# Kernel tuning notes

Measured on AMD Instinct MI355X. Metric: run time of the kernel, lower is better.

Reference implementation:

```python
import jax, jax.numpy as jnp
import numpy as np
from jax import lax

SCORE_THRESHOLD = 0.01
NMS_THRESHOLD = 0.5
MAX_DETECTIONS = 100
PRE_NMS_TOPK = 512  # fixed-shape candidate pool per class (tf NMS is unbounded; 512 >> max_detections covers it)
NEG_INF = -jnp.inf


def setup_inputs() -> dict:
    key = jax.random.key(0)
    k1, k2, k3, k4, k5 = jax.random.split(key, 5)
    B, N, C = 32, 50000, 10
    # valid (x1,y1,x2,y2) boxes: random top-left + positive width/height
    xy = jax.random.uniform(k1, (B, N, 2), dtype=jnp.float32) * 500.0
    wh = jax.random.uniform(k2, (B, N, 2), dtype=jnp.float32) * 100.0 + 1.0
    boxes = jnp.concatenate([xy, xy + wh], axis=-1)
    classification = jax.random.uniform(k3, (B, N, C), dtype=jnp.float32)
    rotation = jax.random.normal(k4, (B, N, 3), dtype=jnp.float32)
    translation = jax.random.normal(k5, (B, N, 3), dtype=jnp.float32)
    return {"boxes": boxes, "classification": classification,
            "rotation": rotation, "translation": translation}


def _iou_matrix(b):  # b: (K,4) in (x1,y1,x2,y2)
    x1, y1, x2, y2 = b[:, 0], b[:, 1], b[:, 2], b[:, 3]
    area = (x2 - x1) * (y2 - y1)  # (K,)
    ix1 = jnp.maximum(x1[:, None], x1[None, :])
    iy1 = jnp.maximum(y1[:, None], y1[None, :])
    ix2 = jnp.minimum(x2[:, None], x2[None, :])
    iy2 = jnp.minimum(y2[:, None], y2[None, :])
    inter = jnp.maximum(ix2 - ix1, 0.0) * jnp.maximum(iy2 - iy1, 0.0)
    union = area[:, None] + area[None, :] - inter
    return jnp.where(union > 0.0, inter / union, 0.0)  # (K,K)


def _greedy_nms_keep(iou, valid):
    # iou: (K,K) for boxes already sorted by descending score; valid: (K,) bool
    K = iou.shape[0]
    def body(suppressed, xs):
        iou_row, valid_i, i = xs
        keep_i = valid_i & jnp.logical_not(suppressed[i])
        suppressed = jnp.where(keep_i, suppressed | (iou_row > NMS_THRESHOLD), suppressed)
        return suppressed, keep_i
    _, keep = lax.scan(body, jnp.zeros((K,), bool), (iou, valid, jnp.arange(K)))
    return keep


def _per_class(scores, boxes_i):
    # scores: (N,), boxes_i: (N,4) -> kept candidate scores (K,) (-inf where dropped) and anchor idx (K,)
    sc = jnp.where(scores > SCORE_THRESHOLD, scores, NEG_INF)
    vals, idx = lax.top_k(sc, PRE_NMS_TOPK)          # sorted desc
    valid = vals > SCORE_THRESHOLD                    # also false for -inf pads
    iou = _iou_matrix(boxes_i[idx])
    keep = _greedy_nms_keep(iou, valid)
    keep = keep & (jnp.cumsum(keep.astype(jnp.int32)) <= MAX_DETECTIONS)
    return jnp.where(keep, vals, NEG_INF), idx


def _per_image(boxes_i, cls_i, rot_i, trans_i):
    # boxes_i (N,4), cls_i (N,C), rot_i (N,3), trans_i (N,3)
    C = cls_i.shape[1]
    sc_ck, idx_ck = jax.vmap(_per_class, in_axes=(1, None))(cls_i, boxes_i)  # (C,K)
    labels_ck = jnp.broadcast_to(jnp.arange(C, dtype=jnp.int32)[:, None], sc_ck.shape)
    sc_flat = sc_ck.reshape(-1)
    idx_flat = idx_ck.reshape(-1)
    lab_flat = labels_ck.reshape(-1)
    top_scores, sel = lax.top_k(sc_flat, MAX_DETECTIONS)   # global top-k across classes
    sel_idx = idx_flat[sel]
    sel_lab = lab_flat[sel]
    valid = jnp.isfinite(top_scores)
    out_boxes = jnp.where(valid[:, None], boxes_i[sel_idx], -1.0)
    out_scores = jnp.where(valid, top_scores, -1.0)
    out_labels = jnp.where(valid, sel_lab, -1).astype(jnp.int32)
    out_rot = jnp.where(valid[:, None], rot_i[sel_idx], -1.0)
    out_trans = jnp.where(valid[:, None], trans_i[sel_idx], -1.0)
    return out_boxes, out_scores, out_labels, out_rot, out_trans


def reference(boxes, classification, rotation, translation):
    return jax.vmap(_per_image)(boxes, classification, rotation, translation)
```

## Files before the change

kernel.cpp:

```cpp
#include <hip/hip_runtime.h>
#include <math.h>

typedef unsigned int u32;
typedef unsigned long long u64;

constexpr int NB   = 32;
constexpr int NN   = 50000;
constexpr int NC   = 10;
constexpr int KK   = 512;
constexpr int MAXD = 100;
constexpr int CAP  = 2048;
constexpr int LCAP = 192;
constexpr int GCH  = 2500;
constexpr int KMAX = 1024;
constexpr u32 TBIN = 252;
constexpr int RLIM = 192;

constexpr int OFF_BOX = 0;
constexpr int OFF_SC  = NB * MAXD * 4;
constexpr int OFF_LB  = OFF_SC + NB * MAXD;
constexpr int OFF_RT  = OFF_LB + NB * MAXD;
constexpr int OFF_TR  = OFF_RT + NB * MAXD * 3;

__device__ __forceinline__ u32 ord_f32(float s) {
  u32 u = __float_as_uint(s);
  return (u & 0x80000000u) ? ~u : (u | 0x80000000u);
}
__device__ __forceinline__ float unord_f32(u32 o) {
  u32 u = (o & 0x80000000u) ? (o & 0x7FFFFFFFu) : ~o;
  return __uint_as_float(u);
}
__device__ __forceinline__ u64 make_key(float s, u32 i) {
  float sp = (s > 0.01f) ? s : -INFINITY;
  return ((u64)ord_f32(sp) << 32) | (u64)(u32)(~i);
}
__device__ __forceinline__ u32 digest16(float x) {
  if (!(x > 0.01f)) return 0;
  u32 q = (u32)(x * 65536.0f);
  return q > 65535u ? 65535u : q;
}
__device__ __forceinline__ float readlane_f(float v, int lane) {
  return __int_as_float(__builtin_amdgcn_readlane(__float_as_int(v), lane));
}
__device__ __forceinline__ u64 readlane_u64(u64 v, int lane) {
  u32 lo = __builtin_amdgcn_readlane((u32)v, lane);
  u32 hi = __builtin_amdgcn_readlane((u32)(v >> 32), lane);
  return ((u64)hi << 32) | lo;
}
__device__ __forceinline__ int clamp_idx(int idx) {
  return idx < 0 ? 0 : (idx >= NN ? NN - 1 : idx);
}

__global__ __launch_bounds__(512) void gather_kernel(
    const float* __restrict__ cls, u64* __restrict__ glist,
    u32* __restrict__ gcnt) {
  const int blk = blockIdx.x;
  const int b = blk / 20, ch = blk % 20;
  const float* src = cls + (size_t)b * NN * NC + (size_t)ch * GCH * NC;
  __shared__ u32 lcnt[NC];
  __shared__ u32 lbase[NC];
  __shared__ u64 lbuf[NC][LCAP];
  const int t = threadIdx.x;
  if (t < NC) lcnt[t] = 0;
  __syncthreads();
  for (int q = t; q < GCH * NC / 4; q += 512) {
    float4 v = ((const float4*)src)[q];
    float arr[4] = {v.x, v.y, v.z, v.w};
#pragma unroll
    for (int k = 0; k < 4; ++k) {
      int e = q * 4 + k;
      int c = e % 10;
      float x = arr[k];
      if ((digest16(x) >> 8) >= TBIN) {
        u32 idx = (u32)((ch * (GCH * NC) + e) / 10);
        u32 p = atomicAdd(&lcnt[c], 1u);
        if (p < (u32)LCAP) {
          lbuf[c][p] = make_key(x, idx);
        } else {
          u32 g = atomicAdd(&gcnt[b * NC + c], 1u);
          if (g < (u32)CAP) glist[(size_t)(b * NC + c) * CAP + g] = make_key(x, idx);
        }
      }
    }
  }
  __syncthreads();
  if (t < NC) {
    u32 n = min(lcnt[t], (u32)LCAP);
    lbase[t] = atomicAdd(&gcnt[b * NC + t], n);
  }
  __syncthreads();
  for (int c = 0; c < NC; ++c) {
    u32 n = min(lcnt[c], (u32)LCAP);
    u32 base = lbase[c];
    for (u32 i = t; i < n; i += 512) {
      u32 p = base + i;
      if (p < (u32)CAP) glist[(size_t)(b * NC + c) * CAP + p] = lbuf[c][i];
    }
  }
}

__global__ __launch_bounds__(512) void sort_kernel(
    const float* __restrict__ cls, const u64* __restrict__ glist,
    const u32* __restrict__ gcnt, const float* __restrict__ boxes,
    u64* __restrict__ selg, float4* __restrict__ bxg) {
  __shared__ __align__(16) unsigned char smem[16448];
  u64* cand = (u64*)smem;
  ushort (*prank)[8] = (ushort(*)[8])(smem + 8192);
  __shared__ int s_cnt, s_d;
  const int p = blockIdx.x >> 1, half = blockIdx.x & 1;
  const int bc = (p & 7) * 40 + (p >> 3);
  const int b = bc / NC;
  const int t = threadIdx.x, lane = t & 63, wv = t >> 6;

  int M = (int)gcnt[bc];
  const bool fast = (M >= KK && M <= KMAX);
  if (fast) {
    for (int i = t; i < KMAX; i += 512)
      cand[i] = (i < M) ? glist[(size_t)bc * CAP + i] : (u64)i;
  } else {
    const int c = bc % NC;
    const float* sbase = cls + (size_t)b * NN * NC + c;
    u32* hist = (u32*)smem;
    for (int i = t; i < 4096; i += 512) hist[i] = 0;
    if (t == 0) s_cnt = 0;
    __syncthreads();
    for (int i = t; i < NN; i += 512)
      atomicAdd(&hist[digest16(sbase[(size_t)i * NC]) >> 4], 1u);
    __syncthreads();
    if (t == 0) {
      u32 run = 0, d = 1;
      for (int i = 4095; i >= 1; --i) {
        run += hist[i];
        if (run >= (u32)KK) { d = (u32)i; break; }
        d = 1;
      }
      s_d = (int)d;
    }
    __syncthreads();
    const u32 dstar = (u32)s_d;
    for (int i = t; i < KMAX; i += 512) cand[i] = (u64)i;
    __syncthreads();
    for (int i = t; i < NN; i += 512) {
      float x = sbase[(size_t)i * NC];
      u32 dg = digest16(x) >> 4;
      if (dg >= dstar && dg >= 1) {
        int pq = atomicAdd(&s_cnt, 1);
        if (pq < KMAX) cand[pq] = make_key(x, (u32)i);
      }
    }
    __syncthreads();
    M = min(s_cnt, KMAX);
  }

  u64 ck0 = 0;
  float4 pb0;
  if (fast) {
    ck0 = cand[half * 512 + t];
    const int pidx = clamp_idx((int)(~(u32)ck0));
    pb0 = *(const float4*)(boxes + ((size_t)b * NN + pidx) * 4);
  }
  __syncthreads();

  const int h2lo = fast ? half : 0;
  const int h2hi = fast ? half : 1;
  for (int h2 = h2lo; h2 <= h2hi; ++h2) {
    {
      u64 myk[8];
#pragma unroll
      for (int k = 0; k < 8; ++k) myk[k] = cand[h2 * 512 + lane + k * 64];
      int rnk[8];
#pragma unroll
      for (int k = 0; k < 8; ++k) rnk[k] = 0;
      const int j0 = wv * 128;
      const int rem = M - j0;
      const int jjmax = rem <= 0 ? 0 : (rem >= 128 ? 64 : ((rem + 1) >> 1));
      for (int jj = 0; jj < jjmax; ++jj) {
        const ulonglong2 v = *(const ulonglong2*)&cand[j0 + jj * 2];
#pragma unroll
        for (int k = 0; k < 8; ++k) {
          rnk[k] += (v.x > myk[k]) ? 1 : 0;
          rnk[k] += (v.y > myk[k]) ? 1 : 0;
        }
      }
#pragma unroll
      for (int k = 0; k < 8; ++k) prank[lane + k * 64][wv] = (ushort)rnk[k];
    }
    __syncthreads();
    {
      const uint4 pv = *(const uint4*)&prank[t][0];
      const int r = (int)(pv.x & 0xFFFFu) + (int)(pv.x >> 16) +
                    (int)(pv.y & 0xFFFFu) + (int)(pv.y >> 16) +
                    (int)(pv.z & 0xFFFFu) + (int)(pv.z >> 16) +
                    (int)(pv.w & 0xFFFFu) + (int)(pv.w >> 16);
      const int ig = h2 * 512 + t;
      if (ig < M && r < KK) {
        const u64 key = fast ? ck0 : cand[ig];
        selg[(size_t)bc * KK + r] = key;
        if (fast) {
          bxg[(size_t)bc * KK + r] = pb0;
        } else {
          const int pidx = clamp_idx((int)(~(u32)key));
          bxg[(size_t)bc * KK + r] =
              *(const float4*)(boxes + ((size_t)b * NN + pidx) * 4);
        }
      }
    }
    if (h2 < h2hi) __syncthreads();
  }
  if (M < KK) {
    for (int r = M + t; r < KK; r += 512) {
      selg[(size_t)bc * KK + r] = make_key(-INFINITY, 0);
      bxg[(size_t)bc * KK + r] =
          *(const float4*)(boxes + ((size_t)b * NN + 0) * 4);
    }
  }
}

__global__ __launch_bounds__(512) void nms_kernel(
    const u64* __restrict__ selg, const float4* __restrict__ bxg,
    int* __restrict__ tidx, float* __restrict__ ksc) {
  __shared__ __align__(16) unsigned char smem[26560];
  float4* bx4 = (float4*)smem;
  float* ars = (float*)(smem + 8192);
  float* sscore = (float*)(smem + 10240);
  u64 (*rowm)[9] = (u64(*)[9])(smem + 12288);
  u64* kmask = (u64*)(smem + 26432);
  const int bc = (blockIdx.x & 7) * 40 + (blockIdx.x >> 3);
  const int t = threadIdx.x, lane = t & 63, wv = t >> 6;

  {
    const u64 k = selg[(size_t)bc * KK + t];
    tidx[bc * KK + t] = clamp_idx((int)(~(u32)k));
    const float4 bx = bxg[(size_t)bc * KK + t];
    bx4[t] = bx;
    ars[t] = (bx.z - bx.x) * (bx.w - bx.y);
    sscore[t] = unord_f32((u32)(k >> 32));
  }
  __syncthreads();

  float jx1[8], jy1[8], jx2[8], jy2[8], jar[8];
#pragma unroll
  for (int q = 0; q < 8; ++q) {
    const float4 bb = bx4[q * 64 + lane];
    jx1[q] = bb.x; jy1[q] = bb.y; jx2[q] = bb.z; jy2[q] = bb.w;
    jar[q] = ars[q * 64 + lane];
  }


#pragma unroll
  for (int g = 0; g < RLIM / 64; ++g) {
    for (int rr = 0; rr < 8; ++rr) {
      const int il = wv + 8 * rr;
      const int i = g * 64 + il;
      const float bix1 = readlane_f(jx1[g], il);
      const float biy1 = readlane_f(jy1[g], il);
      const float bix2 = readlane_f(jx2[g], il);
      const float biy2 = readlane_f(jy2[g], il);
      const float bia  = readlane_f(jar[g], il);
      u64 m[8];
#pragma unroll
      for (int q = 0; q < 8; ++q) {
        m[q] = 0;
        if (q >= g) {
          float ix1 = fmaxf(bix1, jx1[q]);
          float iy1 = fmaxf(biy1, jy1[q]);
          float ix2 = fminf(bix2, jx2[q]);
          float iy2 = fminf(biy2, jy2[q]);
          float iw = fmaxf(ix2 - ix1, 0.0f);
          float ih = fmaxf(iy2 - iy1, 0.0f);
          float inter = iw * ih;
          float uni = bia + jar[q] - inter;
          bool s = (uni > 0.0f) && ((inter - 0.5f * uni) > uni * 0x1p-25f);
          m[q] = __ballot(s);
        }
      }
      u64 word = m[0];
#pragma unroll
      for (int q = 1; q < 8; ++q) word = (lane == q) ? m[q] : word;
      if (lane < 8) rowm[i][lane] = word;
    }
  }
  __syncthreads();

  if (wv == 0) {
    u64 vw_[8], kw[8];
#pragma unroll
    for (int q = 0; q < 8; ++q) {
      const float sc = sscore[q * 64 + lane];
      vw_[q] = __ballot(sc > 0.01f);
      kw[q] = 0;
    }
    u64 vsup = 0;
    int count = 0;
    bool done = false;
#pragma unroll
    for (int w = 0; w < 8; ++w) {
      if (!done) {
        u64 av = vw_[w] & ~readlane_u64(vsup, w);
        while (av) {
          const int bbit = (int)__builtin_ctzll(av);
          const int i = w * 64 + bbit;
          kw[w] |= 1ull << bbit;
          if (++count == MAXD) { done = true; break; }
          if (w < RLIM / 64) {
            const u64 row = (lane < 8) ? rowm[i][lane] : 0;
            vsup |= row;
          } else {
            const float bix1 = readlane_f(jx1[w], bbit);
            const float biy1 = readlane_f(jy1[w], bbit);
            const float bix2 = readlane_f(jx2[w], bbit);
            const float biy2 = readlane_f(jy2[w], bbit);
            const float bia  = readlane_f(jar[w], bbit);
            u64 m[8];
#pragma unroll
            for (int q = 0; q < 8; ++q) {
              m[q] = 0;
              if (q >= w) {
                float ix1 = fmaxf(bix1, jx1[q]);
                float iy1 = fmaxf(biy1, jy1[q]);
                float ix2 = fminf(bix2, jx2[q]);
                float iy2 = fminf(biy2, jy2[q]);
                float iw = fmaxf(ix2 - ix1, 0.0f);
                float ih = fmaxf(iy2 - iy1, 0.0f);
                float inter = iw * ih;
                float uni = bia + jar[q] - inter;
                bool s = (uni > 0.0f) && ((inter - 0.5f * uni) > uni * 0x1p-25f);
                m[q] = __ballot(s);
              }
            }
            u64 word = m[0];
#pragma unroll
            for (int q = 1; q < 8; ++q) word = (lane == q) ? m[q] : word;
            vsup |= word;
          }
          const u64 mask_gt = (bbit == 63) ? 0ull : (~0ull << (bbit + 1));
          av = vw_[w] & ~readlane_u64(vsup, w) & mask_gt;
        }
      }
    }
    if (lane < 8) {
      u64 word = kw[0];
#pragma unroll
      for (int q = 1; q < 8; ++q) word = (lane == q) ? kw[q] : word;
      kmask[lane] = word;
    }
  }
  __syncthreads();
  {
    const float sc = sscore[t];
    const bool keep = (kmask[t >> 6] >> (t & 63)) & 1ull;
    ksc[(size_t)bc * KK + t] = keep ? sc : -INFINITY;
  }
}

__global__ __launch_bounds__(512) void final_kernel(
    const float* __restrict__ boxes, const float* __restrict__ rot,
    const float* __restrict__ trans, const int* __restrict__ tidx,
    const float* __restrict__ ksc, float* __restrict__ out) {
  const int b = blockIdx.x;
  __shared__ __align__(16) u64 ck[KMAX];
  __shared__ __align__(16) ushort prank[KMAX][8];
  __shared__ u64 top[MAXD];
  __shared__ int cnt;
  const int t = threadIdx.x;
  const int lane = t & 63, wv = t >> 6;
  if (t == 0) cnt = 0;
  if (t < MAXD) top[t] = make_key(-INFINITY, 0);
  for (int i = t; i < KMAX; i += 512) ck[i] = (u64)i;
  __syncthreads();
  for (int j = t; j < NC * KK; j += 512) {
    float s = ksc[b * NC * KK + j];
    if (s != -INFINITY) {
      int p = atomicAdd(&cnt, 1);
      if (p < KMAX) ck[p] = ((u64)ord_f32(s) << 32) | (u64)(u32)(~(u32)j);
    }
  }
  __syncthreads();
  const int n = min(cnt, KMAX);
  {
    u64 myk[16];
#pragma unroll
    for (int k = 0; k < 16; ++k) myk[k] = ck[lane + k * 64];
    int rnk[16];
#pragma unroll
    for (int k = 0; k < 16; ++k) rnk[k] = 0;
    const int j0 = wv * 128;
    const int rem = n - j0;
    const int jjmax = rem <= 0 ? 0 : (rem >= 128 ? 64 : ((rem + 1) >> 1));
    for (int jj = 0; jj < jjmax; ++jj) {
      const ulonglong2 v = *(const ulonglong2*)&ck[j0 + jj * 2];
#pragma unroll
      for (int k = 0; k < 16; ++k) {
        rnk[k] += (v.x > myk[k]) ? 1 : 0;
        rnk[k] += (v.y > myk[k]) ? 1 : 0;
      }
    }
#pragma unroll
    for (int k = 0; k < 16; ++k) prank[lane + k * 64][wv] = (ushort)rnk[k];
  }
  __syncthreads();
#pragma unroll
  for (int h = 0; h < 2; ++h) {
    const int i = h * 512 + t;
    const uint4 pv = *(const uint4*)&prank[i][0];
    const int r = (int)(pv.x & 0xFFFFu) + (int)(pv.x >> 16) +
                  (int)(pv.y & 0xFFFFu) + (int)(pv.y >> 16) +
                  (int)(pv.z & 0xFFFFu) + (int)(pv.z >> 16) +
                  (int)(pv.w & 0xFFFFu) + (int)(pv.w >> 16);
    if (i < n && r < MAXD) top[r] = ck[i];
  }
  __syncthreads();

  if (t < MAXD) {
    float b0 = -1.f, b1 = -1.f, b2 = -1.f, b3 = -1.f;
    float os = -1.f, ol = -1.f;
    float r0 = -1.f, r1 = -1.f, r2 = -1.f;
    float t0 = -1.f, t1 = -1.f, t2 = -1.f;
    const u64 k = top[t];
    const float sc = unord_f32((u32)(k >> 32));
    if (sc != -INFINITY) {
      int j = (int)(~(u32)k);
      int c = j >> 9, slot = j & (KK - 1);
      int idx = tidx[(b * NC + c) * KK + slot];
      os = sc;
      ol = (float)c;
      const float4 bx = *(const float4*)(boxes + ((size_t)b * NN + idx) * 4);
      b0 = bx.x; b1 = bx.y; b2 = bx.z; b3 = bx.w;
      const float* rp = rot + ((size_t)b * NN + idx) * 3;
      r0 = rp[0]; r1 = rp[1]; r2 = rp[2];
      const float* tp = trans + ((size_t)b * NN + idx) * 3;
      t0 = tp[0]; t1 = tp[1]; t2 = tp[2];
    }
    const int o = b * MAXD + t;
    out[OFF_BOX + (size_t)o * 4 + 0] = b0;
    out[OFF_BOX + (size_t)o * 4 + 1] = b1;
    out[OFF_BOX + (size_t)o * 4 + 2] = b2;
    out[OFF_BOX + (size_t)o * 4 + 3] = b3;
    out[OFF_SC + o] = os;
    out[OFF_LB + o] = ol;
    out[OFF_RT + (size_t)o * 3 + 0] = r0;
    out[OFF_RT + (size_t)o * 3 + 1] = r1;
    out[OFF_RT + (size_t)o * 3 + 2] = r2;
    out[OFF_TR + (size_t)o * 3 + 0] = t0;
    out[OFF_TR + (size_t)o * 3 + 1] = t1;
    out[OFF_TR + (size_t)o * 3 + 2] = t2;
  }
}

extern "C" void kernel_launch(void* const* d_in, const int* in_sizes, int n_in,
                              void* d_out, int out_size, void* d_ws, size_t ws_size,
                              hipStream_t stream) {
  const float* boxes = (const float*)d_in[0];
  const float* cls   = (const float*)d_in[1];
  const float* rot   = (const float*)d_in[2];
  const float* trans = (const float*)d_in[3];
  float* out = (float*)d_out;

  u64* glist   = (u64*)d_ws;
  u64* selg    = glist + (size_t)NB * NC * CAP;
  float4* bxg  = (float4*)(selg + (size_t)NB * NC * KK);
  int* tidx    = (int*)(bxg + (size_t)NB * NC * KK);
  float* ksc   = (float*)(tidx + NB * NC * KK);
  u32* gcnt    = (u32*)(ksc + NB * NC * KK);

  hipMemsetAsync(gcnt, 0, NB * NC * sizeof(u32), stream);
  gather_kernel<<<NB * 20, 512, 0, stream>>>(cls, glist, gcnt);
  sort_kernel<<<NB * NC * 2, 512, 0, stream>>>(cls, glist, gcnt, boxes, selg, bxg);
  nms_kernel<<<NB * NC, 512, 0, stream>>>(selg, bxg, tidx, ksc);
  final_kernel<<<NB, 512, 0, stream>>>(boxes, rot, trans, tidx, ksc, out);
}
```

Baseline: 111.0 us.

## Replace global atomic compaction with fixed per-chunk segments and drop memset

The gather kernel now writes each chunk's per-class candidates into a fixed 96-slot segment and records a per-chunk count, marking overflow with a sentinel, so global atomics are no longer needed. The sort kernel computes prefix offsets from the 20 chunk counts and compacts the segments into shared memory, falling back to the slow histogram path when any chunk overflows. This removes the hipMemsetAsync launch and global atomic contention. In exchange the sort kernel issues more scattered loads and takes the slow path more often if chunk counts exceed the segment size.

Result: no change. 112.7 us (+1.5%).

```diff
diff --git a/kernel.cpp b/kernel.cpp
--- a/kernel.cpp
+++ b/kernel.cpp
@@ -10,11 +10,13 @@
 constexpr int KK   = 512;
 constexpr int MAXD = 100;
 constexpr int CAP  = 2048;
+constexpr int SEGC = 96;
 constexpr int LCAP = 192;
 constexpr int GCH  = 2500;
 constexpr int KMAX = 1024;
 constexpr u32 TBIN = 252;
 constexpr int RLIM = 192;
+constexpr u32 SENT = 0xFFFFu;
 
 constexpr int OFF_BOX = 0;
 constexpr int OFF_SC  = NB * MAXD * 4;
@@ -53,12 +55,11 @@
 
 __global__ __launch_bounds__(512) void gather_kernel(
     const float* __restrict__ cls, u64* __restrict__ glist,
-    u32* __restrict__ gcnt) {
+    u32* __restrict__ gcnt2) {
   const int blk = blockIdx.x;
   const int b = blk / 20, ch = blk % 20;
   const float* src = cls + (size_t)b * NN * NC + (size_t)ch * GCH * NC;
   __shared__ u32 lcnt[NC];
-  __shared__ u32 lbase[NC];
   __shared__ u64 lbuf[NC][LCAP];
   const int t = threadIdx.x;
   if (t < NC) lcnt[t] = 0;
@@ -74,34 +75,26 @@
       if ((digest16(x) >> 8) >= TBIN) {
         u32 idx = (u32)((ch * (GCH * NC) + e) / 10);
         u32 p = atomicAdd(&lcnt[c], 1u);
-        if (p < (u32)LCAP) {
-          lbuf[c][p] = make_key(x, idx);
-        } else {
-          u32 g = atomicAdd(&gcnt[b * NC + c], 1u);
-          if (g < (u32)CAP) glist[(size_t)(b * NC + c) * CAP + g] = make_key(x, idx);
-        }
+        if (p < (u32)LCAP) lbuf[c][p] = make_key(x, idx);
       }
     }
   }
   __syncthreads();
   if (t < NC) {
-    u32 n = min(lcnt[t], (u32)LCAP);
-    lbase[t] = atomicAdd(&gcnt[b * NC + t], n);
+    u32 n = lcnt[t];
+    gcnt2[(size_t)(b * 20 + ch) * NC + t] = (n > (u32)SEGC) ? SENT : n;
   }
   __syncthreads();
   for (int c = 0; c < NC; ++c) {
-    u32 n = min(lcnt[c], (u32)LCAP);
-    u32 base = lbase[c];
-    for (u32 i = t; i < n; i += 512) {
-      u32 p = base + i;
-      if (p < (u32)CAP) glist[(size_t)(b * NC + c) * CAP + p] = lbuf[c][i];
-    }
+    u32 n = min(lcnt[c], (u32)SEGC);
+    for (u32 i = t; i < n; i += 512)
+      glist[(size_t)(b * NC + c) * CAP + ch * SEGC + i] = lbuf[c][i];
   }
 }
 
 __global__ __launch_bounds__(512) void sort_kernel(
     const float* __restrict__ cls, const u64* __restrict__ glist,
-    const u32* __restrict__ gcnt, const float* __restrict__ boxes,
+    const u32* __restrict__ gcnt2, const float* __restrict__ boxes,
     u64* __restrict__ selg, float4* __restrict__ bxg) {
   __shared__ __align__(16) unsigned char smem[16448];
   u64* cand = (u64*)smem;
@@ -109,16 +102,30 @@
   __shared__ int s_cnt, s_d;
   const int p = blockIdx.x >> 1, half = blockIdx.x & 1;
   const int bc = (p & 7) * 40 + (p >> 3);
-  const int b = bc / NC;
+  const int b = bc / NC, c = bc % NC;
   const int t = threadIdx.x, lane = t & 63, wv = t >> 6;
 
-  int M = (int)gcnt[bc];
-  const bool fast = (M >= KK && M <= KMAX);
+  u32 cnts[20];
+  int pre[20];
+  int M = 0;
+  bool bad = false;
+#pragma unroll
+  for (int s = 0; s < 20; ++s) {
+    u32 n = gcnt2[(size_t)(b * 20 + s) * NC + c];
+    cnts[s] = n;
+    pre[s] = M;
+    if (n == SENT) bad = true; else M += (int)n;
+  }
+  const bool fast = (!bad && M >= KK && M <= KMAX);
   if (fast) {
-    for (int i = t; i < KMAX; i += 512)
-      cand[i] = (i < M) ? glist[(size_t)bc * CAP + i] : (u64)i;
+    for (int i = t; i < KMAX; i += 512) cand[i] = (u64)i;
+    __syncthreads();
+#pragma unroll
+    for (int s = 0; s < 20; ++s) {
+      if (t < (int)cnts[s])
+        cand[pre[s] + t] = glist[(size_t)bc * CAP + s * SEGC + t];
+    }
   } else {
-    const int c = bc % NC;
     const float* sbase = cls + (size_t)b * NN * NC + c;
     u32* hist = (u32*)smem;
     for (int i = t; i < 4096; i += 512) hist[i] = 0;
@@ -151,6 +158,7 @@
     __syncthreads();
     M = min(s_cnt, KMAX);
   }
+  __syncthreads();
 
   u64 ck0 = 0;
   float4 pb0;
@@ -159,7 +167,6 @@
     const int pidx = clamp_idx((int)(~(u32)ck0));
     pb0 = *(const float4*)(boxes + ((size_t)b * NN + pidx) * 4);
   }
-  __syncthreads();
 
   const int h2lo = fast ? half : 0;
   const int h2hi = fast ? half : 1;
@@ -461,11 +468,10 @@
   float4* bxg  = (float4*)(selg + (size_t)NB * NC * KK);
   int* tidx    = (int*)(bxg + (size_t)NB * NC * KK);
   float* ksc   = (float*)(tidx + NB * NC * KK);
-  u32* gcnt    = (u32*)(ksc + NB * NC * KK);
-
-  hipMemsetAsync(gcnt, 0, NB * NC * sizeof(u32), stream);
-  gather_kernel<<<NB * 20, 512, 0, stream>>>(cls, glist, gcnt);
-  sort_kernel<<<NB * NC * 2, 512, 0, stream>>>(cls, glist, gcnt, boxes, selg, bxg);
+  u32* gcnt2   = (u32*)(ksc + NB * NC * KK);
+
+  gather_kernel<<<NB * 20, 512, 0, stream>>>(cls, glist, gcnt2);
+  sort_kernel<<<NB * NC * 2, 512, 0, stream>>>(cls, glist, gcnt2, boxes, selg, bxg);
   nms_kernel<<<NB * NC, 512, 0, stream>>>(selg, bxg, tidx, ksc);
   final_kernel<<<NB, 512, 0, stream>>>(boxes, rot, trans, tidx, ksc, out);
 }
```
